# Kernel optimization log

Hardware: AMD Instinct MI355X
Metric: run time of the kernel (lower is better)

The kernel has to match this reference:

```python
import jax, jax.numpy as jnp
import numpy as np

MAX_DEG = 10  # deepchem GraphConv default max_deg
EPS = 1e-5


def _neighbor_sum(h, adj, deg):
    # h: [B,N,F], adj: [B,N,K] padded neighbor indices, deg: [B,N]
    B = h.shape[0]
    g = h[jnp.arange(B)[:, None, None], adj]  # [B,N,K,F] irregular gather
    mask = (jnp.arange(MAX_DEG)[None, None, :] < deg[:, :, None]).astype(h.dtype)
    return jnp.einsum('bnkf,bnk->bnf', g, mask)


def _graph_conv(h, adj, deg, W_neigh, W_self, b_neigh, b_self):
    # Degree-bucketed conv: atoms of degree d use W_self[d] (and W_neigh[d-1] if d>=1)
    ns = _neighbor_sum(h, adj, deg)  # [B,N,F]
    out = jnp.zeros(h.shape[:-1] + (W_self.shape[-1],), h.dtype)
    for d in range(MAX_DEG + 1):
        m = (deg == d)[..., None].astype(h.dtype)
        t = h @ W_self[d] + b_self[d]
        if d >= 1:
            t = t + ns @ W_neigh[d - 1] + b_neigh[d - 1]
        out = out + m * t
    return out


def _batch_norm(h, gamma, beta):
    # training-mode batch norm over (batch, atom) for each feature channel
    mu = jnp.mean(h, axis=(0, 1), keepdims=True)
    var = jnp.var(h, axis=(0, 1), keepdims=True)
    return (h - mu) * jax.lax.rsqrt(var + EPS) * gamma + beta


def setup_inputs() -> dict:
    key = jax.random.key(0)
    ks = jax.random.split(key, 12)
    B, N, F, H, T = 128, 512, 75, 128, 12
    x = jax.random.normal(ks[0], (B, N, F), dtype=jnp.float32)
    adjacency_list = jax.random.randint(ks[1], (B, N, MAX_DEG), 0, N)
    degree_list = jax.random.randint(ks[2], (B, N), 0, MAX_DEG + 1)
    s1 = 1.0 / np.sqrt(F)
    s2 = 1.0 / np.sqrt(H)
    return {
        'x': x,
        'adjacency_list': adjacency_list,
        'degree_list': degree_list,
        'W_neigh1': jax.random.normal(ks[3], (MAX_DEG, F, H), dtype=jnp.float32) * s1,
        'W_self1': jax.random.normal(ks[4], (MAX_DEG + 1, F, H), dtype=jnp.float32) * s1,
        'b_neigh1': jnp.zeros((MAX_DEG, H), jnp.float32),
        'b_self1': jnp.zeros((MAX_DEG + 1, H), jnp.float32),
        'gamma1': jnp.ones((H,), jnp.float32),
        'beta1': jnp.zeros((H,), jnp.float32),
        'W_neigh2': jax.random.normal(ks[5], (MAX_DEG, H, H), dtype=jnp.float32) * s2,
        'W_self2': jax.random.normal(ks[6], (MAX_DEG + 1, H, H), dtype=jnp.float32) * s2,
        'b_neigh2': jnp.zeros((MAX_DEG, H), jnp.float32),
        'b_self2': jnp.zeros((MAX_DEG + 1, H), jnp.float32),
        'gamma2': jnp.ones((H,), jnp.float32),
        'beta2': jnp.zeros((H,), jnp.float32),
        'W_dense': jax.random.normal(ks[7], (H, T), dtype=jnp.float32) * s2,
        'b_dense': jnp.zeros((T,), jnp.float32),
    }


def reference(x, adjacency_list, degree_list,
              W_neigh1, W_self1, b_neigh1, b_self1, gamma1, beta1,
              W_neigh2, W_self2, b_neigh2, b_self2, gamma2, beta2,
              W_dense, b_dense):
    h = _graph_conv(x, adjacency_list, degree_list, W_neigh1, W_self1, b_neigh1, b_self1)
    h = jax.nn.relu(_batch_norm(h, gamma1, beta1))
    h = _graph_conv(h, adjacency_list, degree_list, W_neigh2, W_self2, b_neigh2, b_self2)
    h = jax.nn.relu(_batch_norm(h, gamma2, beta2))
    # dropout is identity at inference
    h = jnp.mean(h, axis=1)  # graph-level mean pool over atoms -> [B,H]
    return h @ W_dense + b_dense  # [B, n_tasks]
```

## Files before the change

### kernel.cpp

```cpp
#include <hip/hip_runtime.h>

#define NODES   65536
#define NGRAPH  512
#define BATCH   128
#define HID     128
#define TOUT    12
#define MAXDEG  10
#define NDEG    11
#define EPSV    1e-5f
#define MT      128
#define NTILES  (NODES / MT + NDEG)
#define PCAP    544

typedef float f32x4 __attribute__((ext_vector_type(4)));

__device__ __forceinline__ f32x4 ntload(const float* p) {
    return __builtin_nontemporal_load((const f32x4*)p);
}
__device__ __forceinline__ void ntstore(float* p, f32x4 v) {
    __builtin_nontemporal_store(v, (f32x4*)p);
}
__device__ __forceinline__ f32x4 bnrelu4(f32x4 v, f32x4 sc, f32x4 sh) {
    f32x4 r;
    r.x = fmaxf(fmaf(v.x, sc.x, sh.x), 0.f);
    r.y = fmaxf(fmaf(v.y, sc.y, sh.y), 0.f);
    r.z = fmaxf(fmaf(v.z, sc.z, sh.z), 0.f);
    r.w = fmaxf(fmaf(v.w, sc.w, sh.w), 0.f);
    return r;
}

__global__ void k_zero(f32x4* part4, float* stats1, float* stats2, int* cnt) {
    int i = blockIdx.x * 256 + threadIdx.x;
    part4[i] = 0.f;
    if (blockIdx.x == 0) {
        stats1[threadIdx.x] = 0.f;
        stats2[threadIdx.x] = 0.f;
        if (threadIdx.x < 16) cnt[threadIdx.x] = 0;
    }
}

__global__ void k_bucket(const int* __restrict__ deg, int* __restrict__ cnt,
                         int* __restrict__ lists) {
    __shared__ int s_cnt[NDEG];
    __shared__ int s_base[NDEG];
    int t = threadIdx.x;
    if (t < NDEG) s_cnt[t] = 0;
    __syncthreads();
    int i = blockIdx.x * 256 + t;
    int d = deg[i];
    d = d < 0 ? 0 : (d > MAXDEG ? MAXDEG : d);
    int pos = atomicAdd(&s_cnt[d], 1);
    __syncthreads();
    if (t < NDEG) s_base[t] = atomicAdd(&cnt[t], s_cnt[t]);
    __syncthreads();
    lists[d * NODES + s_base[d] + pos] = i;
}

__global__ void k_plan(const int* __restrict__ cnt, int* __restrict__ offs) {
    if (threadIdx.x == 0) {
        int acc = 0;
        offs[0] = 0;
        for (int d = 0; d < NDEG; ++d) {
            acc += (cnt[d] + MT - 1) / MT;
            offs[d + 1] = acc;
        }
    }
}

__global__ void k_build1(const float* __restrict__ Ws, const float* __restrict__ Wn,
                         float* __restrict__ Wcat) {
    int idx = blockIdx.x * 256 + threadIdx.x;
    int h4 = idx & 31;
    int k  = (idx >> 5) % 160;
    int d  = idx / (160 * 32);
    f32x4 v = 0.f;
    if (k < 75)
        v = *(const f32x4*)(Ws + ((size_t)d * 75 + k) * 128 + h4 * 4);
    else if (k >= 80 && k < 155 && d >= 1)
        v = *(const f32x4*)(Wn + ((size_t)(d - 1) * 75 + (k - 80)) * 128 + h4 * 4);
    *(f32x4*)(Wcat + ((size_t)d * 160 + k) * 128 + h4 * 4) = v;
}
__global__ void k_build2(const float* __restrict__ Ws, const float* __restrict__ Wn,
                         float* __restrict__ Wcat) {
    int idx = blockIdx.x * 256 + threadIdx.x;
    int h4 = idx & 31;
    int k  = (idx >> 5) & 255;
    int d  = idx >> 13;
    f32x4 v = 0.f;
    if (k < 128)
        v = *(const f32x4*)(Ws + ((size_t)d * 128 + k) * 128 + h4 * 4);
    else if (d >= 1)
        v = *(const f32x4*)(Wn + ((size_t)(d - 1) * 128 + (k - 128)) * 128 + h4 * 4);
    *(f32x4*)(Wcat + ((size_t)d * 256 + k) * 128 + h4 * 4) = v;
}
__global__ void k_bias(const float* bs1, const float* bn1, const float* bs2, const float* bn2,
                       float* bcat1, float* bcat2) {
    int d = blockIdx.x, t = threadIdx.x;
    if (t < 128) bcat1[d * 128 + t] = bs1[d * 128 + t] + (d > 0 ? bn1[(d - 1) * 128 + t] : 0.f);
    else { int h = t - 128; bcat2[d * 128 + h] = bs2[d * 128 + h] + (d > 0 ? bn2[(d - 1) * 128 + h] : 0.f); }
}

__global__ void k_ns1(const float* __restrict__ x, const int* __restrict__ adj,
                      const int* __restrict__ deg, float* __restrict__ feats1) {
    int idx = blockIdx.x * 256 + threadIdx.x;
    int node = idx / 20;
    int q = idx - node * 20;
    int f = q * 4;
    int d = deg[node];
    d = d < 0 ? 0 : (d > MAXDEG ? MAXDEG : d);
    const int* arow = adj + node * MAXDEG;
    int base = node & ~(NGRAPH - 1);
    f32x4 s = 0.f;
    for (int k = 0; k < d; ++k) {
        const float* xr = x + (size_t)(base + arow[k]) * 75 + f;
        if (f + 3 < 75) { s.x += xr[0]; s.y += xr[1]; s.z += xr[2]; s.w += xr[3]; }
        else {
            if (f + 0 < 75) s.x += xr[0];
            if (f + 1 < 75) s.y += xr[1];
            if (f + 2 < 75) s.z += xr[2];
        }
    }
    *(f32x4*)(feats1 + (size_t)node * 160 + 80 + f) = s;
    f32x4 v = 0.f;
    const float* xs = x + (size_t)node * 75 + f;
    if (f + 3 < 75) { v.x = xs[0]; v.y = xs[1]; v.z = xs[2]; v.w = xs[3]; }
    else {
        if (f + 0 < 75) v.x = xs[0];
        if (f + 1 < 75) v.y = xs[1];
        if (f + 2 < 75) v.z = xs[2];
    }
    *(f32x4*)(feats1 + (size_t)node * 160 + f) = v;
}

__global__ void k_scale(const float* __restrict__ stats, const float* __restrict__ g,
                        const float* __restrict__ be, float* __restrict__ sc,
                        float* __restrict__ sh) {
    int c = threadIdx.x;
    const float inv = 1.f / (float)NODES;
    float mu  = stats[c] * inv;
    float var = stats[HID + c] * inv - mu * mu;
    float rs  = rsqrtf(var + EPSV);
    float s   = g[c] * rs;
    sc[c] = s;
    sh[c] = be[c] - mu * s;
}

__global__ void k_ns2(const float* __restrict__ h1, const int* __restrict__ adj,
                      const int* __restrict__ deg, const float* __restrict__ sc,
                      const float* __restrict__ sh, float* __restrict__ ns2) {
    int idx = blockIdx.x * 256 + threadIdx.x;
    int node = idx >> 5;
    int f = (idx & 31) * 4;
    int d = deg[node];
    d = d < 0 ? 0 : (d > MAXDEG ? MAXDEG : d);
    const int* arow = adj + node * MAXDEG;
    int base = node & ~(NGRAPH - 1);
    f32x4 sc4 = *(const f32x4*)(sc + f);
    f32x4 sh4 = *(const f32x4*)(sh + f);
    f32x4 s = 0.f;
    for (int k = 0; k < d; ++k) {
        f32x4 v = *(const f32x4*)(h1 + (size_t)(base + arow[k]) * HID + f);
        s += bnrelu4(v, sc4, sh4);
    }
    *(f32x4*)(ns2 + (size_t)node * HID + f) = s;
}

template<int S, bool BN>
__global__ __launch_bounds__(256, 2)
void k_conv(const float* __restrict__ f160, const float* __restrict__ h1,
            const float* __restrict__ ns2, const float* __restrict__ Wcat,
            const float* __restrict__ bcat, const float* __restrict__ sc,
            const float* __restrict__ sh, const int* __restrict__ lists,
            const int* __restrict__ cnt, const int* __restrict__ offs,
            float* __restrict__ out, float* __restrict__ partials) {
    constexpr int NCH = S / 16;

    __shared__ int   s_ids[MT];
    __shared__ float sW[2][16][128];
    __shared__ float sF[2][16][132];

    const int bid = blockIdx.x;
    if (bid >= offs[NDEG]) return;
    int d = 0;
    #pragma unroll
    for (int q = 1; q < NDEG; ++q) d += (bid >= offs[q]);
    const int c  = cnt[d];
    const int m0 = (bid - offs[d]) * MT;
    const int mv = min(MT, c - m0);
    const int t  = threadIdx.x;

    if (t < MT) s_ids[t] = lists[d * NODES + m0 + (t < mv ? t : 0)];
    __syncthreads();

    const int kw = t >> 4;
    const int cw = (t & 15) * 8;
    const int fr = t >> 1;
    const int k8 = (t & 1) * 8;
    const float* Wbase = Wcat + (size_t)d * S * 128;
    const int fid = s_ids[fr];
    const float* Frow1 = (S == 160) ? (f160 + (size_t)fid * 160) : nullptr;
    const float* FrowS = (S == 256) ? (h1 + (size_t)fid * 128) : nullptr;
    const float* FrowN = (S == 256) ? (ns2 + (size_t)fid * 128) : nullptr;

    f32x4 w0, w1, f0, f1;
    auto LOAD = [&](int ch) {
        const float* wp = Wbase + (size_t)(ch * 16 + kw) * 128 + cw;
        w0 = *(const f32x4*)(wp);
        w1 = *(const f32x4*)(wp + 4);
        if constexpr (S == 160) {
            const float* fp = Frow1 + ch * 16 + k8;
            f0 = ntload(fp);
            f1 = ntload(fp + 4);
        } else {
            if (ch < 8) {
                const float* fp = FrowS + ch * 16 + k8;
                f0 = ntload(fp);
                f1 = ntload(fp + 4);
                if constexpr (BN) {
                    int cc = ch * 16 + k8;
                    f0 = bnrelu4(f0, *(const f32x4*)(sc + cc), *(const f32x4*)(sh + cc));
                    f1 = bnrelu4(f1, *(const f32x4*)(sc + cc + 4), *(const f32x4*)(sh + cc + 4));
                }
            } else {
                const float* fp = FrowN + (ch - 8) * 16 + k8;
                f0 = ntload(fp);
                f1 = ntload(fp + 4);
            }
        }
    };
    auto STORE = [&](int buf) {
        *(f32x4*)&sW[buf][kw][cw]     = w0;
        *(f32x4*)&sW[buf][kw][cw + 4] = w1;
        sF[buf][k8 + 0][fr] = f0.x; sF[buf][k8 + 1][fr] = f0.y;
        sF[buf][k8 + 2][fr] = f0.z; sF[buf][k8 + 3][fr] = f0.w;
        sF[buf][k8 + 4][fr] = f1.x; sF[buf][k8 + 5][fr] = f1.y;
        sF[buf][k8 + 6][fr] = f1.z; sF[buf][k8 + 7][fr] = f1.w;
    };

    const int cg = t & 15;
    const int rg = t >> 4;

    f32x4 acc[8][2];
    {
        f32x4 b0 = *(const f32x4*)(bcat + d * HID + cg * 8);
        f32x4 b1 = *(const f32x4*)(bcat + d * HID + cg * 8 + 4);
        #pragma unroll
        for (int j = 0; j < 8; ++j) { acc[j][0] = b0; acc[j][1] = b1; }
    }

    LOAD(0); STORE(0);
    __syncthreads();

    for (int ch = 0; ch < NCH; ++ch) {
        const int buf = ch & 1;
        const bool more = (ch + 1 < NCH);
        if (more) LOAD(ch + 1);
        #pragma unroll 4
        for (int k = 0; k < 16; ++k) {
            f32x4 wA = *(const f32x4*)&sW[buf][k][cg * 8];
            f32x4 wB = *(const f32x4*)&sW[buf][k][cg * 8 + 4];
            f32x4 fA = *(const f32x4*)&sF[buf][k][rg * 8];
            f32x4 fB = *(const f32x4*)&sF[buf][k][rg * 8 + 4];
            acc[0][0] += fA.x * wA;  acc[0][1] += fA.x * wB;
            acc[1][0] += fA.y * wA;  acc[1][1] += fA.y * wB;
            acc[2][0] += fA.z * wA;  acc[2][1] += fA.z * wB;
            acc[3][0] += fA.w * wA;  acc[3][1] += fA.w * wB;
            acc[4][0] += fB.x * wA;  acc[4][1] += fB.x * wB;
            acc[5][0] += fB.y * wA;  acc[5][1] += fB.y * wB;
            acc[6][0] += fB.z * wA;  acc[6][1] += fB.z * wB;
            acc[7][0] += fB.w * wA;  acc[7][1] += fB.w * wB;
        }
        if (more) STORE(buf ^ 1);
        __syncthreads();
    }

    f32x4 cs0 = 0.f, cs1 = 0.f, cq0 = 0.f, cq1 = 0.f;
    #pragma unroll
    for (int j = 0; j < 8; ++j) {
        int i = rg * 8 + j;
        if (i < mv) {
            float* op = out + (size_t)s_ids[i] * HID + cg * 8;
            ntstore(op, acc[j][0]);
            ntstore(op + 4, acc[j][1]);
            cs0 += acc[j][0]; cs1 += acc[j][1];
            cq0 += acc[j][0] * acc[j][0]; cq1 += acc[j][1] * acc[j][1];
        }
    }
    __syncthreads();
    float* red = &sW[0][0][0];
    *(f32x4*)&red[rg * 256 + cg * 8]           = cs0;
    *(f32x4*)&red[rg * 256 + cg * 8 + 4]       = cs1;
    *(f32x4*)&red[rg * 256 + 128 + cg * 8]     = cq0;
    *(f32x4*)&red[rg * 256 + 128 + cg * 8 + 4] = cq1;
    __syncthreads();
    {
        float tot = 0.f;
        #pragma unroll
        for (int g = 0; g < 16; ++g) tot += red[g * 256 + t];
        partials[(size_t)bid * 256 + t] = tot;
    }
}

__global__ void k_redstats(float* __restrict__ partials, float* __restrict__ stats) {
    int t = threadIdx.x;
    float acc = 0.f;
    for (int bx = blockIdx.x; bx < PCAP; bx += gridDim.x) {
        float* p = partials + (size_t)bx * 256 + t;
        acc += *p;
        *p = 0.f;
    }
    atomicAdd(&stats[t], acc);
}

__global__ void k_pool_dense(const float* __restrict__ h2, const float* __restrict__ stats,
                             const float* __restrict__ gamma, const float* __restrict__ beta,
                             const float* __restrict__ Wd, const float* __restrict__ bd,
                             float* __restrict__ outp) {
    __shared__ float s_part[4][HID];
    __shared__ float s_pool[HID];
    const int b = blockIdx.x;
    const int t = threadIdx.x;
    const int hcol = t & (HID - 1);
    const int q = t >> 7;
    const float inv = 1.f / (float)NODES;
    float mu  = stats[hcol] * inv;
    float var = stats[HID + hcol] * inv - mu * mu;
    float rs  = rsqrtf(var + EPSV);
    float sc  = gamma[hcol] * rs;
    float sh  = beta[hcol] - mu * sc;
    float acc = 0.f;
    const float* hp = h2 + ((size_t)b * NGRAPH + q * 128) * HID + hcol;
    #pragma unroll 4
    for (int n = 0; n < 128; ++n)
        acc += fmaxf(fmaf(hp[(size_t)n * HID], sc, sh), 0.f);
    s_part[q][hcol] = acc;
    __syncthreads();
    if (t < HID)
        s_pool[t] = (s_part[0][t] + s_part[1][t] + s_part[2][t] + s_part[3][t]) * (1.f / NGRAPH);
    __syncthreads();
    if (t < TOUT) {
        float o = bd[t];
        for (int hh = 0; hh < HID; ++hh)
            o = fmaf(s_pool[hh], Wd[hh * TOUT + t], o);
        outp[b * TOUT + t] = o;
    }
}

extern "C" void kernel_launch(void* const* d_in, const int* in_sizes, int n_in,
                              void* d_out, int out_size, void* d_ws, size_t ws_size,
                              hipStream_t stream) {
    const float* x   = (const float*)d_in[0];
    const int*   adj = (const int*)d_in[1];
    const int*   deg = (const int*)d_in[2];
    const float* Wn1 = (const float*)d_in[3];
    const float* Ws1 = (const float*)d_in[4];
    const float* bn1 = (const float*)d_in[5];
    const float* bs1 = (const float*)d_in[6];
    const float* g1  = (const float*)d_in[7];
    const float* be1 = (const float*)d_in[8];
    const float* Wn2 = (const float*)d_in[9];
    const float* Ws2 = (const float*)d_in[10];
    const float* bn2 = (const float*)d_in[11];
    const float* bs2 = (const float*)d_in[12];
    const float* g2  = (const float*)d_in[13];
    const float* be2 = (const float*)d_in[14];
    const float* Wd  = (const float*)d_in[15];
    const float* bd  = (const float*)d_in[16];

    float* ws     = (float*)d_ws;
    float* feats1 = ws;
    float* h2     = ws;
    float* h1     = ws + 10485760;
    float* ns2    = ws + 18874368;
    float* Wcat1  = ws + 27262976;
    float* Wcat2  = ws + 27488256;
    float* bcat1  = ws + 27848704;
    float* bcat2  = ws + 27850112;
    float* part   = ws + 27851520;
    float* stats1 = ws + 27990784;
    float* stats2 = ws + 27991040;
    float* sc1    = ws + 27991296;
    float* sh1    = ws + 27991424;
    int*   cnt    = (int*)(ws + 27991552);
    int*   offs   = cnt + 16;
    int*   lists  = cnt + 32;

    k_zero<<<PCAP / 4, 256, 0, stream>>>((f32x4*)part, stats1, stats2, cnt);
    k_bucket<<<NODES / 256, 256, 0, stream>>>(deg, cnt, lists);
    k_plan<<<1, 64, 0, stream>>>(cnt, offs);
    k_build1<<<220, 256, 0, stream>>>(Ws1, Wn1, Wcat1);
    k_build2<<<352, 256, 0, stream>>>(Ws2, Wn2, Wcat2);
    k_bias<<<NDEG, 256, 0, stream>>>(bs1, bn1, bs2, bn2, bcat1, bcat2);

    k_ns1<<<NODES * 20 / 256, 256, 0, stream>>>(x, adj, deg, feats1);
    k_conv<160, false><<<NTILES, 256, 0, stream>>>(feats1, nullptr, nullptr, Wcat1, bcat1,
                                                   nullptr, nullptr, lists, cnt, offs,
                                                   h1, part);
    k_redstats<<<32, 256, 0, stream>>>(part, stats1);
    k_scale<<<1, 128, 0, stream>>>(stats1, g1, be1, sc1, sh1);

    k_ns2<<<8192, 256, 0, stream>>>(h1, adj, deg, sc1, sh1, ns2);
    k_conv<256, true><<<NTILES, 256, 0, stream>>>(nullptr, h1, ns2, Wcat2, bcat2,
                                                  sc1, sh1, lists, cnt, offs,
                                                  h2, part);
    k_redstats<<<32, 256, 0, stream>>>(part, stats2);

    k_pool_dense<<<BATCH, 512, 0, stream>>>(h2, stats2, g2, be2, Wd, bd, (float*)d_out);
}
```

Measured before the change: 345.0 us.

## Halve conv row tile to 64 and remap threads for higher occupancy

Shrinks the per-block node tile in the degree-bucketed conv GEMM from 128 to 64 rows. Each thread now computes an 8x4 output patch instead of 8x8, and loads are remapped so each wave owns a 32-column slice. Launch bounds go from 2 to 6 blocks per SM and workspace offsets move to fit the larger partials buffer. The aim is more blocks and waves in flight to hide gather and global-load latency, at the cost of lower arithmetic intensity per LDS read, more blocks, and more partial-statistics rows to reduce.

```diff
diff --git a/kernel.cpp b/kernel.cpp
--- a/kernel.cpp
+++ b/kernel.cpp
@@ -8,9 +8,9 @@
 #define MAXDEG  10
 #define NDEG    11
 #define EPSV    1e-5f
-#define MT      128
+#define MT      64
 #define NTILES  (NODES / MT + NDEG)
-#define PCAP    544
+#define PCAP    1056
 
 typedef float f32x4 __attribute__((ext_vector_type(4)));
 
@@ -166,7 +166,7 @@
 }
 
 template<int S, bool BN>
-__global__ __launch_bounds__(256, 2)
+__global__ __launch_bounds__(256, 6)
 void k_conv(const float* __restrict__ f160, const float* __restrict__ h1,
             const float* __restrict__ ns2, const float* __restrict__ Wcat,
             const float* __restrict__ bcat, const float* __restrict__ sc,
@@ -177,7 +177,7 @@
 
     __shared__ int   s_ids[MT];
     __shared__ float sW[2][16][128];
-    __shared__ float sF[2][16][132];
+    __shared__ float sF[2][16][68];
 
     const int bid = blockIdx.x;
     if (bid >= offs[NDEG]) return;
@@ -192,60 +192,55 @@
     if (t < MT) s_ids[t] = lists[d * NODES + m0 + (t < mv ? t : 0)];
     __syncthreads();
 
-    const int kw = t >> 4;
-    const int cw = (t & 15) * 8;
-    const int fr = t >> 1;
-    const int k8 = (t & 1) * 8;
+    const int kw = t >> 5;
+    const int c4 = t & 31;
+    const int fr = t >> 2;
+    const int kq = t & 3;
     const float* Wbase = Wcat + (size_t)d * S * 128;
     const int fid = s_ids[fr];
     const float* Frow1 = (S == 160) ? (f160 + (size_t)fid * 160) : nullptr;
     const float* FrowS = (S == 256) ? (h1 + (size_t)fid * 128) : nullptr;
     const float* FrowN = (S == 256) ? (ns2 + (size_t)fid * 128) : nullptr;
 
-    f32x4 w0, w1, f0, f1;
+    f32x4 w0, w1, f0;
     auto LOAD = [&](int ch) {
-        const float* wp = Wbase + (size_t)(ch * 16 + kw) * 128 + cw;
+        const float* wp = Wbase + (size_t)(ch * 16 + kw) * 128 + c4 * 4;
         w0 = *(const f32x4*)(wp);
-        w1 = *(const f32x4*)(wp + 4);
+        w1 = *(const f32x4*)(wp + 8 * 128);
         if constexpr (S == 160) {
-            const float* fp = Frow1 + ch * 16 + k8;
-            f0 = ntload(fp);
-            f1 = ntload(fp + 4);
+            f0 = ntload(Frow1 + ch * 16 + kq * 4);
         } else {
             if (ch < 8) {
-                const float* fp = FrowS + ch * 16 + k8;
-                f0 = ntload(fp);
-                f1 = ntload(fp + 4);
-                if constexpr (BN) {
-                    int cc = ch * 16 + k8;
+                int cc = ch * 16 + kq * 4;
+                f0 = ntload(FrowS + cc);
+                if constexpr (BN)
                     f0 = bnrelu4(f0, *(const f32x4*)(sc + cc), *(const f32x4*)(sh + cc));
-                    f1 = bnrelu4(f1, *(const f32x4*)(sc + cc + 4), *(const f32x4*)(sh + cc + 4));
-                }
             } else {
-                const float* fp = FrowN + (ch - 8) * 16 + k8;
-                f0 = ntload(fp);
-                f1 = ntload(fp + 4);
+                f0 = ntload(FrowN + (ch - 8) * 16 + kq * 4);
             }
         }
     };
     auto STORE = [&](int buf) {
-        *(f32x4*)&sW[buf][kw][cw]     = w0;
-        *(f32x4*)&sW[buf][kw][cw + 4] = w1;
-        sF[buf][k8 + 0][fr] = f0.x; sF[buf][k8 + 1][fr] = f0.y;
-        sF[buf][k8 + 2][fr] = f0.z; sF[buf][k8 + 3][fr] = f0.w;
-        sF[buf][k8 + 4][fr] = f1.x; sF[buf][k8 + 5][fr] = f1.y;
-        sF[buf][k8 + 6][fr] = f1.z; sF[buf][k8 + 7][fr] = f1.w;
+        *(f32x4*)&sW[buf][kw][c4 * 4]     = w0;
+        *(f32x4*)&sW[buf][kw + 8][c4 * 4] = w1;
+        sF[buf][kq * 4 + 0][fr] = f0.x;
+        sF[buf][kq * 4 + 1][fr] = f0.y;
+        sF[buf][kq * 4 + 2][fr] = f0.z;
+        sF[buf][kq * 4 + 3][fr] = f0.w;
     };
 
-    const int cg = t & 15;
-    const int rg = t >> 4;
-
-    f32x4 acc[8][2];
+    const int wave = t >> 6;
+    const int lane = t & 63;
+    const int ccg  = lane & 7;
+    const int rrg  = lane >> 3;
+    const int colb = wave * 32 + ccg * 4;
+    const int rowb = rrg * 8;
+
+    f32x4 acc[8];
     {
-        f32x4 b0 = *(const f32x4*)(bcat + d * HID + cg * 8);
-        f32x4 b1 = *(const f32x4*)(bcat + d * HID + cg * 8 + 4);
+        f32x4 b = *(const f32x4*)(bcat + d * HID + colb);
         #pragma unroll
-        for (int j = 0; j < 8; ++j) { acc[j][0] = b0; acc[j][1] = b1; }
+        for (int j = 0; j < 8; ++j) acc[j] = b;
     }
 
     LOAD(0); STORE(0);
@@ -255,48 +250,43 @@
         const int buf = ch & 1;
         const bool more = (ch + 1 < NCH);
         if (more) LOAD(ch + 1);
-        #pragma unroll 4
+        #pragma unroll 8
         for (int k = 0; k < 16; ++k) {
-            f32x4 wA = *(const f32x4*)&sW[buf][k][cg * 8];
-            f32x4 wB = *(const f32x4*)&sW[buf][k][cg * 8 + 4];
-            f32x4 fA = *(const f32x4*)&sF[buf][k][rg * 8];
-            f32x4 fB = *(const f32x4*)&sF[buf][k][rg * 8 + 4];
-            acc[0][0] += fA.x * wA;  acc[0][1] += fA.x * wB;
-            acc[1][0] += fA.y * wA;  acc[1][1] += fA.y * wB;
-            acc[2][0] += fA.z * wA;  acc[2][1] += fA.z * wB;
-            acc[3][0] += fA.w * wA;  acc[3][1] += fA.w * wB;
-            acc[4][0] += fB.x * wA;  acc[4][1] += fB.x * wB;
-            acc[5][0] += fB.y * wA;  acc[5][1] += fB.y * wB;
-            acc[6][0] += fB.z * wA;  acc[6][1] += fB.z * wB;
-            acc[7][0] += fB.w * wA;  acc[7][1] += fB.w * wB;
+            f32x4 wv = *(const f32x4*)&sW[buf][k][colb];
+            f32x4 fA = *(const f32x4*)&sF[buf][k][rowb];
+            f32x4 fB = *(const f32x4*)&sF[buf][k][rowb + 4];
+            acc[0] += fA.x * wv;
+            acc[1] += fA.y * wv;
+            acc[2] += fA.z * wv;
+            acc[3] += fA.w * wv;
+            acc[4] += fB.x * wv;
+            acc[5] += fB.y * wv;
+            acc[6] += fB.z * wv;
+            acc[7] += fB.w * wv;
         }
         if (more) STORE(buf ^ 1);
         __syncthreads();
     }
 
-    f32x4 cs0 = 0.f, cs1 = 0.f, cq0 = 0.f, cq1 = 0.f;
+    f32x4 cs = 0.f, cq = 0.f;
     #pragma unroll
     for (int j = 0; j < 8; ++j) {
-        int i = rg * 8 + j;
+        int i = rowb + j;
         if (i < mv) {
-            float* op = out + (size_t)s_ids[i] * HID + cg * 8;
-            ntstore(op, acc[j][0]);
-            ntstore(op + 4, acc[j][1]);
-            cs0 += acc[j][0]; cs1 += acc[j][1];
-            cq0 += acc[j][0] * acc[j][0]; cq1 += acc[j][1] * acc[j][1];
+            ntstore(out + (size_t)s_ids[i] * HID + colb, acc[j]);
+            cs += acc[j];
+            cq += acc[j] * acc[j];
         }
     }
     __syncthreads();
     float* red = &sW[0][0][0];
-    *(f32x4*)&red[rg * 256 + cg * 8]           = cs0;
-    *(f32x4*)&red[rg * 256 + cg * 8 + 4]       = cs1;
-    *(f32x4*)&red[rg * 256 + 128 + cg * 8]     = cq0;
-    *(f32x4*)&red[rg * 256 + 128 + cg * 8 + 4] = cq1;
+    *(f32x4*)&red[rrg * 256 + colb]       = cs;
+    *(f32x4*)&red[rrg * 256 + 128 + colb] = cq;
     __syncthreads();
     {
         float tot = 0.f;
         #pragma unroll
-        for (int g = 0; g < 16; ++g) tot += red[g * 256 + t];
+        for (int g = 0; g < 8; ++g) tot += red[g * 256 + t];
         partials[(size_t)bid * 256 + t] = tot;
     }
 }
@@ -377,11 +367,11 @@
     float* bcat1  = ws + 27848704;
     float* bcat2  = ws + 27850112;
     float* part   = ws + 27851520;
-    float* stats1 = ws + 27990784;
-    float* stats2 = ws + 27991040;
-    float* sc1    = ws + 27991296;
-    float* sh1    = ws + 27991424;
-    int*   cnt    = (int*)(ws + 27991552);
+    float* stats1 = ws + 28121856;
+    float* stats2 = ws + 28122112;
+    float* sc1    = ws + 28122368;
+    float* sh1    = ws + 28122496;
+    int*   cnt    = (int*)(ws + 28122624);
     int*   offs   = cnt + 16;
     int*   lists  = cnt + 32;
 
```

New measurement: 347.8 us. About the same (+0.8%).
